# Optimization experiments

Measured on AMD Instinct MI355X. Metric: run time of the kernel, lower is better.

## Reference

```python
import jax, jax.numpy as jnp
import numpy as np

NUM_HEADS = 16
HEAD_DIM = 64
WINDOW = 512
D_MODEL = NUM_HEADS * HEAD_DIM
BATCH = 2
SEQ = 2048


def setup_inputs() -> dict:
    key = jax.random.key(0)
    k1, k2, k3 = jax.random.split(key, 3)
    x = jax.random.normal(k1, (BATCH, SEQ, D_MODEL), dtype=jnp.float32)
    # Dense layer params (lecun_normal-like scale for stability)
    qkv_kernel = jax.random.normal(k2, (D_MODEL, 3 * NUM_HEADS * HEAD_DIM), dtype=jnp.float32) / np.sqrt(D_MODEL)
    qkv_bias = jnp.zeros((3 * NUM_HEADS * HEAD_DIM,), dtype=jnp.float32)
    out_kernel = jax.random.normal(k3, (NUM_HEADS * HEAD_DIM, D_MODEL), dtype=jnp.float32) / np.sqrt(D_MODEL)
    out_bias = jnp.zeros((D_MODEL,), dtype=jnp.float32)
    return {"x": x, "qkv_kernel": qkv_kernel, "qkv_bias": qkv_bias,
            "out_kernel": out_kernel, "out_bias": out_bias}


def reference(x, qkv_kernel, qkv_bias, out_kernel, out_bias):
    b, s, d = x.shape
    qkv = x @ qkv_kernel + qkv_bias                       # (b, s, 3*H*hd)
    qkv = qkv.reshape(b, s, 3, NUM_HEADS, HEAD_DIM)
    q = qkv[:, :, 0].transpose(0, 2, 1, 3)                # (b, H, s, hd)
    k = qkv[:, :, 1].transpose(0, 2, 1, 3)
    v = qkv[:, :, 2].transpose(0, 2, 1, 3)
    scale = 1.0 / jnp.sqrt(jnp.float32(HEAD_DIM)).astype(x.dtype)
    scores = jnp.einsum('bhqd,bhkd->bhqk', q, k) * scale  # (b, H, s, s)
    rows = jnp.arange(s)[:, None]
    cols = jnp.arange(s)[None, :]
    window_mask = (rows - cols >= 0) & (rows - cols < WINDOW)
    scores = jnp.where(window_mask[None, None], scores, jnp.asarray(-1e9, scores.dtype))
    attn = jax.nn.softmax(scores, axis=-1)
    out = jnp.einsum('bhqk,bhkd->bhqd', attn, v)          # (b, H, s, hd)
    out = out.transpose(0, 2, 1, 3).reshape(b, s, -1)
    return out @ out_kernel + out_bias
```

## Files before the change

kernel.cpp:

```cpp
#include <hip/hip_runtime.h>
#include <cstdint>
#include <cstddef>

#define NUM_HEADS 16
#define HEAD_DIM  64
#define WINDOW    512
#define D_MODEL   1024
#define BATCH     2
#define SEQ       2048
#define MTOT      (BATCH*SEQ)
#define NQKV      (3*D_MODEL)

typedef short bf16x8 __attribute__((ext_vector_type(8)));
typedef float f32x4  __attribute__((ext_vector_type(4)));

__device__ __forceinline__ f32x4 mfma16(bf16x8 a, bf16x8 b, f32x4 c) {
  return __builtin_amdgcn_mfma_f32_16x16x32_bf16(a, b, c, 0, 0, 0);
}

__device__ __forceinline__ unsigned short f2bf(float f) {
  unsigned int u = __float_as_uint(f);
  u += 0x7fffu + ((u >> 16) & 1u);
  return (unsigned short)(u >> 16);
}
__device__ __forceinline__ float bf2f(unsigned short b) {
  return __uint_as_float(((unsigned int)b) << 16);
}

__device__ __forceinline__ void gld16(const unsigned short* g, unsigned short* l) {
  __builtin_amdgcn_global_load_lds(
      (const __attribute__((address_space(1))) unsigned int*)g,
      (__attribute__((address_space(3))) unsigned int*)l, 16, 0, 0);
}

__global__ __launch_bounds__(256) void prep_kernel(const float* __restrict__ x,
                                                   const float* __restrict__ qkv_w,
                                                   const float* __restrict__ out_w,
                                                   unsigned short* __restrict__ Xb,
                                                   unsigned short* __restrict__ Wq,
                                                   unsigned short* __restrict__ Wo) {
  __shared__ float tile[32][33];
  const int bid = blockIdx.x, t = threadIdx.x;
  if (bid < 4096) {
    int i = (bid * 256 + t) * 4;
    float4 v = *(const float4*)(x + i);
    ushort4 o;
    o.x = f2bf(v.x); o.y = f2bf(v.y); o.z = f2bf(v.z); o.w = f2bf(v.w);
    *(ushort4*)(Xb + i) = o;
    return;
  }
  const float* in; unsigned short* out; int R, C, bx, by;
  if (bid < 7168) { int b2 = bid - 4096; in = qkv_w; out = Wq; R = D_MODEL; C = NQKV; bx = b2 % 96; by = b2 / 96; }
  else            { int b2 = bid - 7168; in = out_w; out = Wo; R = D_MODEL; C = D_MODEL; bx = b2 & 31; by = b2 >> 5; }
  int tx = t & 31, ty = t >> 5;
  int c0 = bx * 32, r0 = by * 32;
#pragma unroll
  for (int i = 0; i < 32; i += 8)
    tile[ty + i][tx] = in[(size_t)(r0 + ty + i) * C + c0 + tx];
  __syncthreads();
#pragma unroll
  for (int i = 0; i < 32; i += 8)
    out[(size_t)(c0 + ty + i) * R + r0 + tx] = f2bf(tile[tx][ty + i]);
}

template<int TI, bool SWAP>
__device__ __forceinline__ void gemm_mainloop_db(const unsigned short* __restrict__ A,
                                                 const unsigned short* __restrict__ Bt,
                                                 int K, int m0, int n0,
                                                 unsigned short* sA0, unsigned short* sA1,
                                                 unsigned short* sB0, unsigned short* sB1,
                                                 f32x4 (&acc)[TI][4]) {
  const int t = threadIdx.x;
  const int lane = t & 63, wave = t >> 6;
  const int wm = wave >> 1, wn = wave & 1;
  const int lhi = lane >> 4, llo = lane & 15;
  f32x4 zero = {0.f, 0.f, 0.f, 0.f};
#pragma unroll
  for (int i = 0; i < TI; ++i)
#pragma unroll
    for (int j = 0; j < 4; ++j) acc[i][j] = zero;

  const int cswz = (((t & 3) ^ ((t >> 3) & 3)) << 3);
  const unsigned short* gA = A  + (size_t)(m0 + (t >> 2)) * K + cswz;
  const unsigned short* gB = Bt + (size_t)(n0 + (t >> 2)) * K + cswz;
  const size_t rowskip = (size_t)64 * K;
  const int ldsT = t * 8;
  const int rsw  = (lhi ^ ((llo >> 1) & 3)) * 8;
  const int aoff = (wm * (TI * 16) + llo) * 32 + rsw;
  const int boff = (wn * 64 + llo) * 32 + rsw;

  gld16(gA, sA0 + ldsT);
  if (TI == 4) gld16(gA + rowskip, sA0 + ldsT + 2048);
  gld16(gB, sB0 + ldsT);
  gld16(gB + rowskip, sB0 + ldsT + 2048);

  const int nIter = K >> 5;
  for (int it = 0; it < nIter; ++it) {
    __syncthreads();
    unsigned short* cA = (it & 1) ? sA1 : sA0;
    unsigned short* cB = (it & 1) ? sB1 : sB0;
    if (it + 1 < nIter) {
      unsigned short* nA = (it & 1) ? sA0 : sA1;
      unsigned short* nB = (it & 1) ? sB0 : sB1;
      gA += 32; gB += 32;
      gld16(gA, nA + ldsT);
      if (TI == 4) gld16(gA + rowskip, nA + ldsT + 2048);
      gld16(gB, nB + ldsT);
      gld16(gB + rowskip, nB + ldsT + 2048);
    }
    bf16x8 af[TI], bfr[4];
#pragma unroll
    for (int i = 0; i < TI; ++i) af[i]  = *(const bf16x8*)(cA + aoff + i * 512);
#pragma unroll
    for (int j = 0; j < 4; ++j)  bfr[j] = *(const bf16x8*)(cB + boff + j * 512);
#pragma unroll
    for (int i = 0; i < TI; ++i)
#pragma unroll
      for (int j = 0; j < 4; ++j)
        acc[i][j] = SWAP ? mfma16(bfr[j], af[i], acc[i][j])
                         : mfma16(af[i], bfr[j], acc[i][j]);
  }
}

__global__ __launch_bounds__(256) void qkv_gemm_kernel(const unsigned short* __restrict__ Xb,
                                                       const unsigned short* __restrict__ Wt,
                                                       const float* __restrict__ bias,
                                                       unsigned short* __restrict__ Qw,
                                                       unsigned short* __restrict__ Kw,
                                                       unsigned short* __restrict__ Vtw) {
  __shared__ __align__(16) unsigned short sA[2][128 * 32];
  __shared__ __align__(16) unsigned short sB[2][128 * 32];
  f32x4 acc[4][4];
  const int m0 = blockIdx.y * 128, n0 = blockIdx.x * 128;
  const int t = threadIdx.x, lane = t & 63, wave = t >> 6;
  const int wm = wave >> 1, wn = wave & 1, lhi = lane >> 4, llo = lane & 15;

  if (n0 < 2048) {
    gemm_mainloop_db<4, false>(Xb, Wt, D_MODEL, m0, n0, sA[0], sA[1], sB[0], sB[1], acc);
#pragma unroll
    for (int ti = 0; ti < 4; ++ti) {
#pragma unroll
      for (int tj = 0; tj < 4; ++tj) {
        int n = n0 + wn * 64 + tj * 16 + llo;
        float bv = bias[n];
        int c = n >> 10, h = (n >> 6) & 15, d = n & 63;
#pragma unroll
        for (int r = 0; r < 4; ++r) {
          int m = m0 + wm * 64 + ti * 16 + lhi * 4 + r;
          int b = m >> 11, s = m & 2047;
          int bh = b * 16 + h;
          float v = acc[ti][tj][r] + bv;
          size_t idx = ((size_t)(bh * 2048 + s)) * 64 + d;
          if (c == 0) Qw[idx] = f2bf(v * 0.125f);
          else        Kw[idx] = f2bf(v);
        }
      }
    }
  } else {
    gemm_mainloop_db<4, true>(Xb, Wt, D_MODEL, m0, n0, sA[0], sA[1], sB[0], sB[1], acc);
#pragma unroll
    for (int ti = 0; ti < 4; ++ti) {
      int m = m0 + wm * 64 + ti * 16 + llo;
      int b = m >> 11, s = m & 2047;
#pragma unroll
      for (int tj = 0; tj < 4; ++tj) {
        int nb = n0 + wn * 64 + tj * 16 + lhi * 4;
        float4 bv = *(const float4*)(bias + nb);
        int h = (nb >> 6) & 15, dbase = nb & 63;
        int bh = b * 16 + h;
        float bvr[4] = {bv.x, bv.y, bv.z, bv.w};
#pragma unroll
        for (int r = 0; r < 4; ++r)
          Vtw[(size_t)(bh * 64 + dbase + r) * 2048 + s] = f2bf(acc[ti][tj][r] + bvr[r]);
      }
    }
  }
}

__global__ __launch_bounds__(256) void attn_kernel(const unsigned short* __restrict__ Qw,
                                                   const unsigned short* __restrict__ Kw,
                                                   const unsigned short* __restrict__ Vtw,
                                                   unsigned short* __restrict__ AO) {
  __shared__ __align__(16) unsigned short sK[2][64 * 64];
  __shared__ __align__(16) unsigned short sV[2][64 * 64];
  __shared__ __align__(16) unsigned short sP[4][16 * 72];
  const int t = threadIdx.x, lane = t & 63, wave = t >> 6;
  const int lhi = lane >> 4, llo = lane & 15;
  const int bh = blockIdx.x;
  const int q0 = (31 - blockIdx.y) << 6;
  const unsigned short* Qb = Qw  + (size_t)bh * 2048 * 64;
  const unsigned short* Kb = Kw  + (size_t)bh * 2048 * 64;
  const unsigned short* Vb = Vtw + (size_t)bh * 64 * 2048;

  const int qrow = q0 + wave * 16 + llo;
  bf16x8 qf0 = *(const bf16x8*)(Qb + (size_t)qrow * 64 + lhi * 8);
  bf16x8 qf1 = *(const bf16x8*)(Qb + (size_t)qrow * 64 + 32 + lhi * 8);

  const int srow = t >> 3;
  const int scol = ((t & 7) ^ (srow & 7)) * 8;
  const int cpos  = (lhi ^ (llo & 7)) * 8;
  const int cposx = cpos ^ 32;

  float m_i = -1e30f, l_i = 0.f;
  f32x4 o[4];
  f32x4 zero = {0.f, 0.f, 0.f, 0.f};
#pragma unroll
  for (int td = 0; td < 4; ++td) o[td] = zero;

  const int kt_lo = (q0 > 511) ? ((q0 - 511) >> 6) : 0;
  const int kt_hi = q0 >> 6;

  {
    const int k0 = kt_lo << 6;
    unsigned short* dK = sK[kt_lo & 1];
    unsigned short* dV = sV[kt_lo & 1];
    gld16(Kb + (size_t)(k0 + srow) * 64 + scol,      dK + t * 8);
    gld16(Kb + (size_t)(k0 + srow + 32) * 64 + scol, dK + t * 8 + 2048);
    gld16(Vb + (size_t)srow * 2048 + k0 + scol,        dV + t * 8);
    gld16(Vb + (size_t)(srow + 32) * 2048 + k0 + scol, dV + t * 8 + 2048);
  }

  for (int kt = kt_lo; kt <= kt_hi; ++kt) {
    __syncthreads();
    if (kt < kt_hi) {
      const int k0n = (kt + 1) << 6;
      unsigned short* dK = sK[(kt + 1) & 1];
      unsigned short* dV = sV[(kt + 1) & 1];
      gld16(Kb + (size_t)(k0n + srow) * 64 + scol,      dK + t * 8);
      gld16(Kb + (size_t)(k0n + srow + 32) * 64 + scol, dK + t * 8 + 2048);
      gld16(Vb + (size_t)srow * 2048 + k0n + scol,        dV + t * 8);
      gld16(Vb + (size_t)(srow + 32) * 2048 + k0n + scol, dV + t * 8 + 2048);
    }
    const unsigned short* bK = sK[kt & 1];
    const unsigned short* bV = sV[kt & 1];
    const int k0 = kt << 6;

    f32x4 st[4];
#pragma unroll
    for (int tk = 0; tk < 4; ++tk) {
      const unsigned short* kr = bK + (tk * 16 + llo) * 64;
      bf16x8 kf0 = *(const bf16x8*)(kr + cpos);
      bf16x8 kf1 = *(const bf16x8*)(kr + cposx);
      f32x4 z = zero;
      z = mfma16(kf0, qf0, z);
      z = mfma16(kf1, qf1, z);
      st[tk] = z;
    }

    const int kb = k0 + lhi * 4;
    float mx = -1e30f;
#pragma unroll
    for (int tk = 0; tk < 4; ++tk)
#pragma unroll
      for (int r = 0; r < 4; ++r) {
        int key = kb + tk * 16 + r;
        bool ok = (key <= qrow) && (qrow - key < WINDOW);
        float s = ok ? st[tk][r] : -1e30f;
        st[tk][r] = s;
        mx = fmaxf(mx, s);
      }
    mx = fmaxf(mx, __shfl_xor(mx, 16));
    mx = fmaxf(mx, __shfl_xor(mx, 32));
    float mn = fmaxf(m_i, mx);
    float a  = __expf(m_i - mn);
    float rs = 0.f;
    unsigned short* pw = &sP[wave][llo * 72];
#pragma unroll
    for (int tk = 0; tk < 4; ++tk) {
      ushort4 pb;
      pb.x = f2bf(__expf(st[tk][0] - mn));
      pb.y = f2bf(__expf(st[tk][1] - mn));
      pb.z = f2bf(__expf(st[tk][2] - mn));
      pb.w = f2bf(__expf(st[tk][3] - mn));
      *(ushort4*)(pw + tk * 16 + lhi * 4) = pb;
      rs += bf2f(pb.x) + bf2f(pb.y) + bf2f(pb.z) + bf2f(pb.w);
    }
    rs += __shfl_xor(rs, 16);
    rs += __shfl_xor(rs, 32);
    l_i = l_i * a + rs;
    m_i = mn;

    float aR[4];
#pragma unroll
    for (int r = 0; r < 4; ++r) aR[r] = __shfl(a, lhi * 4 + r);
#pragma unroll
    for (int td = 0; td < 4; ++td)
#pragma unroll
      for (int r = 0; r < 4; ++r) o[td][r] *= aR[r];

    bf16x8 pf0 = *(const bf16x8*)(pw + lhi * 8);
    bf16x8 pf1 = *(const bf16x8*)(pw + 32 + lhi * 8);
#pragma unroll
    for (int td = 0; td < 4; ++td) {
      const unsigned short* vr = bV + (td * 16 + llo) * 64;
      bf16x8 vf0 = *(const bf16x8*)(vr + cpos);
      bf16x8 vf1 = *(const bf16x8*)(vr + cposx);
      o[td] = mfma16(pf0, vf0, o[td]);
      o[td] = mfma16(pf1, vf1, o[td]);
    }
  }

  float lR[4];
#pragma unroll
  for (int r = 0; r < 4; ++r) lR[r] = 1.f / __shfl(l_i, lhi * 4 + r);
  const int b = bh >> 4, h = bh & 15;
#pragma unroll
  for (int td = 0; td < 4; ++td)
#pragma unroll
    for (int r = 0; r < 4; ++r) {
      int qr = q0 + wave * 16 + lhi * 4 + r;
      AO[(size_t)(b * 2048 + qr) * 1024 + h * 64 + td * 16 + llo] = f2bf(o[td][r] * lR[r]);
    }
}

__global__ __launch_bounds__(256) void out_gemm_kernel(const unsigned short* __restrict__ AO,
                                                       const unsigned short* __restrict__ Wt,
                                                       const float* __restrict__ bias,
                                                       float* __restrict__ out) {
  __shared__ __align__(16) unsigned short sA[2][64 * 32];
  __shared__ __align__(16) unsigned short sB[2][128 * 32];
  f32x4 acc[2][4];
  const int m0 = blockIdx.y * 64, n0 = blockIdx.x * 128;
  gemm_mainloop_db<2, false>(AO, Wt, D_MODEL, m0, n0, sA[0], sA[1], sB[0], sB[1], acc);

  const int t = threadIdx.x, lane = t & 63, wave = t >> 6;
  const int wm = wave >> 1, wn = wave & 1, lhi = lane >> 4, llo = lane & 15;
#pragma unroll
  for (int ti = 0; ti < 2; ++ti)
#pragma unroll
    for (int tj = 0; tj < 4; ++tj) {
      int n = n0 + wn * 64 + tj * 16 + llo;
      float bv = bias[n];
#pragma unroll
      for (int r = 0; r < 4; ++r) {
        int m = m0 + wm * 32 + ti * 16 + lhi * 4 + r;
        out[(size_t)m * D_MODEL + n] = acc[ti][tj][r] + bv;
      }
    }
}

extern "C" void kernel_launch(void* const* d_in, const int* in_sizes, int n_in,
                              void* d_out, int out_size, void* d_ws, size_t ws_size,
                              hipStream_t stream) {
  const float* x      = (const float*)d_in[0];
  const float* qkv_w  = (const float*)d_in[1];
  const float* qkv_b  = (const float*)d_in[2];
  const float* out_w  = (const float*)d_in[3];
  const float* out_b  = (const float*)d_in[4];
  float* out = (float*)d_out;
  char* ws = (char*)d_ws;

  unsigned short* Xb  = (unsigned short*)(ws);
  unsigned short* Wq  = (unsigned short*)(ws + ((size_t)8  << 20));
  unsigned short* Wo  = (unsigned short*)(ws + ((size_t)14 << 20));
  unsigned short* Qw  = (unsigned short*)(ws + ((size_t)16 << 20));
  unsigned short* Kw  = (unsigned short*)(ws + ((size_t)24 << 20));
  unsigned short* Vtw = (unsigned short*)(ws + ((size_t)32 << 20));
  unsigned short* AO  = (unsigned short*)(ws + ((size_t)40 << 20));

  prep_kernel<<<8192, 256, 0, stream>>>(x, qkv_w, out_w, Xb, Wq, Wo);
  qkv_gemm_kernel<<<dim3(NQKV / 128, MTOT / 128), 256, 0, stream>>>(Xb, Wq, qkv_b, Qw, Kw, Vtw);
  attn_kernel<<<dim3(BATCH * NUM_HEADS, SEQ / 64), 256, 0, stream>>>(Qw, Kw, Vtw, AO);
  out_gemm_kernel<<<dim3(D_MODEL / 128, MTOT / 64), 256, 0, stream>>>(AO, Wo, out_b, out);
}
```

Baseline: 172.5 us.

## Double attention query tile to 128 rows with 512 threads, unroll GEMM pipeline

The attention kernel now processes 128 query rows per block with 8 waves, so each K/V tile staged in LDS serves twice as many queries. Each thread loads half as much per tile, and waves skip tiles outside their own causal window. The GEMM mainloop is restructured into a two-step unrolled ping-pong that drops per-iteration buffer selection, and the QKV epilogue hoists the Q/K destination and scale choice out of the loop. A wave that skips a tile stalls at the next barrier, and using fewer blocks may lower occupancy and balance.

Result: slower. 186.0 us (+7.8%).

```diff
diff --git a/kernel.cpp b/kernel.cpp
--- a/kernel.cpp
+++ b/kernel.cpp
@@ -63,6 +63,32 @@
     out[(size_t)(c0 + ty + i) * R + r0 + tx] = f2bf(tile[tx][ty + i]);
 }
 
+template<int TI>
+__device__ __forceinline__ void stage_tile(const unsigned short* gA, const unsigned short* gB,
+                                           size_t rowskip, int ldsT,
+                                           unsigned short* dA, unsigned short* dB) {
+  gld16(gA, dA + ldsT);
+  if (TI == 4) gld16(gA + rowskip, dA + ldsT + 2048);
+  gld16(gB, dB + ldsT);
+  gld16(gB + rowskip, dB + ldsT + 2048);
+}
+
+template<int TI, bool SWAP>
+__device__ __forceinline__ void compute_tile(const unsigned short* cA, const unsigned short* cB,
+                                             int aoff, int boff, f32x4 (&acc)[TI][4]) {
+  bf16x8 af[TI], bfr[4];
+#pragma unroll
+  for (int i = 0; i < TI; ++i) af[i]  = *(const bf16x8*)(cA + aoff + i * 512);
+#pragma unroll
+  for (int j = 0; j < 4; ++j)  bfr[j] = *(const bf16x8*)(cB + boff + j * 512);
+#pragma unroll
+  for (int i = 0; i < TI; ++i)
+#pragma unroll
+    for (int j = 0; j < 4; ++j)
+      acc[i][j] = SWAP ? mfma16(bfr[j], af[i], acc[i][j])
+                       : mfma16(af[i], bfr[j], acc[i][j]);
+}
+
 template<int TI, bool SWAP>
 __device__ __forceinline__ void gemm_mainloop_db(const unsigned short* __restrict__ A,
                                                  const unsigned short* __restrict__ Bt,
@@ -89,36 +115,18 @@
   const int aoff = (wm * (TI * 16) + llo) * 32 + rsw;
   const int boff = (wn * 64 + llo) * 32 + rsw;
 
-  gld16(gA, sA0 + ldsT);
-  if (TI == 4) gld16(gA + rowskip, sA0 + ldsT + 2048);
-  gld16(gB, sB0 + ldsT);
-  gld16(gB + rowskip, sB0 + ldsT + 2048);
-
+  stage_tile<TI>(gA, gB, rowskip, ldsT, sA0, sB0);
   const int nIter = K >> 5;
-  for (int it = 0; it < nIter; ++it) {
+#pragma unroll 1
+  for (int it = 0; it < nIter; it += 2) {
+    gA += 32; gB += 32;
     __syncthreads();
-    unsigned short* cA = (it & 1) ? sA1 : sA0;
-    unsigned short* cB = (it & 1) ? sB1 : sB0;
-    if (it + 1 < nIter) {
-      unsigned short* nA = (it & 1) ? sA0 : sA1;
-      unsigned short* nB = (it & 1) ? sB0 : sB1;
-      gA += 32; gB += 32;
-      gld16(gA, nA + ldsT);
-      if (TI == 4) gld16(gA + rowskip, nA + ldsT + 2048);
-      gld16(gB, nB + ldsT);
-      gld16(gB + rowskip, nB + ldsT + 2048);
-    }
-    bf16x8 af[TI], bfr[4];
-#pragma unroll
-    for (int i = 0; i < TI; ++i) af[i]  = *(const bf16x8*)(cA + aoff + i * 512);
-#pragma unroll
-    for (int j = 0; j < 4; ++j)  bfr[j] = *(const bf16x8*)(cB + boff + j * 512);
-#pragma unroll
-    for (int i = 0; i < TI; ++i)
-#pragma unroll
-      for (int j = 0; j < 4; ++j)
-        acc[i][j] = SWAP ? mfma16(bfr[j], af[i], acc[i][j])
-                         : mfma16(af[i], bfr[j], acc[i][j]);
+    if (it + 1 < nIter) stage_tile<TI>(gA, gB, rowskip, ldsT, sA1, sB1);
+    compute_tile<TI, SWAP>(sA0, sB0, aoff, boff, acc);
+    gA += 32; gB += 32;
+    __syncthreads();
+    if (it + 2 < nIter) stage_tile<TI>(gA, gB, rowskip, ldsT, sA0, sB0);
+    if (it + 1 < nIter) compute_tile<TI, SWAP>(sA1, sB1, aoff, boff, acc);
   }
 }
 
@@ -137,22 +145,22 @@
 
   if (n0 < 2048) {
     gemm_mainloop_db<4, false>(Xb, Wt, D_MODEL, m0, n0, sA[0], sA[1], sB[0], sB[1], acc);
+    const int c = n0 >> 10;
+    unsigned short* __restrict__ Dst = (c == 0) ? Qw : Kw;
+    const float qscale = (c == 0) ? 0.125f : 1.0f;
 #pragma unroll
     for (int ti = 0; ti < 4; ++ti) {
 #pragma unroll
       for (int tj = 0; tj < 4; ++tj) {
         int n = n0 + wn * 64 + tj * 16 + llo;
         float bv = bias[n];
-        int c = n >> 10, h = (n >> 6) & 15, d = n & 63;
+        int h = (n >> 6) & 15, d = n & 63;
 #pragma unroll
         for (int r = 0; r < 4; ++r) {
           int m = m0 + wm * 64 + ti * 16 + lhi * 4 + r;
           int b = m >> 11, s = m & 2047;
           int bh = b * 16 + h;
-          float v = acc[ti][tj][r] + bv;
-          size_t idx = ((size_t)(bh * 2048 + s)) * 64 + d;
-          if (c == 0) Qw[idx] = f2bf(v * 0.125f);
-          else        Kw[idx] = f2bf(v);
+          Dst[((size_t)(bh * 2048 + s)) * 64 + d] = f2bf((acc[ti][tj][r] + bv) * qscale);
         }
       }
     }
@@ -177,22 +185,23 @@
   }
 }
 
-__global__ __launch_bounds__(256) void attn_kernel(const unsigned short* __restrict__ Qw,
+__global__ __launch_bounds__(512) void attn_kernel(const unsigned short* __restrict__ Qw,
                                                    const unsigned short* __restrict__ Kw,
                                                    const unsigned short* __restrict__ Vtw,
                                                    unsigned short* __restrict__ AO) {
   __shared__ __align__(16) unsigned short sK[2][64 * 64];
   __shared__ __align__(16) unsigned short sV[2][64 * 64];
-  __shared__ __align__(16) unsigned short sP[4][16 * 72];
+  __shared__ __align__(16) unsigned short sP[8][16 * 72];
   const int t = threadIdx.x, lane = t & 63, wave = t >> 6;
   const int lhi = lane >> 4, llo = lane & 15;
   const int bh = blockIdx.x;
-  const int q0 = (31 - blockIdx.y) << 6;
+  const int q0 = (15 - blockIdx.y) << 7;
   const unsigned short* Qb = Qw  + (size_t)bh * 2048 * 64;
   const unsigned short* Kb = Kw  + (size_t)bh * 2048 * 64;
   const unsigned short* Vb = Vtw + (size_t)bh * 64 * 2048;
 
-  const int qrow = q0 + wave * 16 + llo;
+  const int qw = q0 + wave * 16;
+  const int qrow = qw + llo;
   bf16x8 qf0 = *(const bf16x8*)(Qb + (size_t)qrow * 64 + lhi * 8);
   bf16x8 qf1 = *(const bf16x8*)(Qb + (size_t)qrow * 64 + 32 + lhi * 8);
 
@@ -208,16 +217,14 @@
   for (int td = 0; td < 4; ++td) o[td] = zero;
 
   const int kt_lo = (q0 > 511) ? ((q0 - 511) >> 6) : 0;
-  const int kt_hi = q0 >> 6;
+  const int kt_hi = (q0 + 127) >> 6;
 
   {
     const int k0 = kt_lo << 6;
     unsigned short* dK = sK[kt_lo & 1];
     unsigned short* dV = sV[kt_lo & 1];
-    gld16(Kb + (size_t)(k0 + srow) * 64 + scol,      dK + t * 8);
-    gld16(Kb + (size_t)(k0 + srow + 32) * 64 + scol, dK + t * 8 + 2048);
-    gld16(Vb + (size_t)srow * 2048 + k0 + scol,        dV + t * 8);
-    gld16(Vb + (size_t)(srow + 32) * 2048 + k0 + scol, dV + t * 8 + 2048);
+    gld16(Kb + (size_t)(k0 + srow) * 64 + scol, dK + t * 8);
+    gld16(Vb + (size_t)srow * 2048 + k0 + scol, dV + t * 8);
   }
 
   for (int kt = kt_lo; kt <= kt_hi; ++kt) {
@@ -226,14 +233,14 @@
       const int k0n = (kt + 1) << 6;
       unsigned short* dK = sK[(kt + 1) & 1];
       unsigned short* dV = sV[(kt + 1) & 1];
-      gld16(Kb + (size_t)(k0n + srow) * 64 + scol,      dK + t * 8);
-      gld16(Kb + (size_t)(k0n + srow + 32) * 64 + scol, dK + t * 8 + 2048);
-      gld16(Vb + (size_t)srow * 2048 + k0n + scol,        dV + t * 8);
-      gld16(Vb + (size_t)(srow + 32) * 2048 + k0n + scol, dV + t * 8 + 2048);
-    }
+      gld16(Kb + (size_t)(k0n + srow) * 64 + scol, dK + t * 8);
+      gld16(Vb + (size_t)srow * 2048 + k0n + scol, dV + t * 8);
+    }
+    const int k0 = kt << 6;
+    if (k0 > qw + 15 || k0 + 63 < qw - (WINDOW - 1)) continue;
+
     const unsigned short* bK = sK[kt & 1];
     const unsigned short* bV = sV[kt & 1];
-    const int k0 = kt << 6;
 
     f32x4 st[4];
 #pragma unroll
@@ -360,6 +367,6 @@
 
   prep_kernel<<<8192, 256, 0, stream>>>(x, qkv_w, out_w, Xb, Wq, Wo);
   qkv_gemm_kernel<<<dim3(NQKV / 128, MTOT / 128), 256, 0, stream>>>(Xb, Wq, qkv_b, Qw, Kw, Vtw);
-  attn_kernel<<<dim3(BATCH * NUM_HEADS, SEQ / 64), 256, 0, stream>>>(Qw, Kw, Vtw, AO);
+  attn_kernel<<<dim3(BATCH * NUM_HEADS, SEQ / 128), 512, 0, stream>>>(Qw, Kw, Vtw, AO);
   out_gemm_kernel<<<dim3(D_MODEL / 128, MTOT / 64), 256, 0, stream>>>(AO, Wo, out_b, out);
 }
```
